# Kernel tuning notes

Measured on AMD Instinct MI355X. Metric: run time of the kernel, lower is better.

The kernel has to match this reference:

```python
import jax, jax.numpy as jnp
import numpy as np


def _lstm_cell(x, h, c, W_ih, W_hh, b_ih, b_hh):
    # torch gate order: input, forget, cell(g), output
    g = x @ W_ih.T + h @ W_hh.T + b_ih + b_hh
    i, f, gg, o = jnp.split(g, 4, axis=-1)
    c_new = jax.nn.sigmoid(f) * c + jax.nn.sigmoid(i) * jnp.tanh(gg)
    h_new = jax.nn.sigmoid(o) * jnp.tanh(c_new)
    return h_new, c_new


def setup_inputs() -> dict:
    key = jax.random.key(0)
    ks = jax.random.split(key, 11)
    T, B, D, E, H, V = 64, 4096, 32, 32, 5, 10
    IN = D + 3 * E  # 128 = input_size
    s = 0.1
    return {
        "horizon": T,
        "hidden": jax.random.normal(ks[0], (2, B, H), jnp.float32),
        "cell": jax.random.normal(ks[1], (2, B, H), jnp.float32),
        "dec_x": jax.random.normal(ks[2], (T, B, D), jnp.float32),
        "mote_id_cat": jax.random.randint(ks[3], (T, B), 0, V),
        "fault_type_cat": jax.random.randint(ks[4], (T, B), 0, V),
        "mote_fault_cat": jax.random.randint(ks[5], (T, B), 0, V),
        "mote_embed": jax.random.normal(ks[6], (V, E), jnp.float32),
        "W_ih0": jax.random.normal(ks[7], (4 * H, IN), jnp.float32) * s,
        "W_hh0": jax.random.normal(ks[8], (4 * H, H), jnp.float32) * s,
        "b_ih0": jnp.zeros((4 * H,), jnp.float32),
        "b_hh0": jnp.zeros((4 * H,), jnp.float32),
        "W_ih1": jax.random.normal(ks[9], (4 * H, H), jnp.float32) * s,
        "W_hh1": jax.random.normal(ks[10], (4 * H, H), jnp.float32) * s,
        "b_ih1": jnp.zeros((4 * H,), jnp.float32),
        "b_hh1": jnp.zeros((4 * H,), jnp.float32),
    }


def reference(horizon, hidden, cell, dec_x, mote_id_cat, fault_type_cat,
              mote_fault_cat, mote_embed, W_ih0, W_hh0, b_ih0, b_hh0,
              W_ih1, W_hh1, b_ih1, b_hh1):
    # Faithful to source: ALL three categorical features use mote_embed.
    e1 = mote_embed[mote_id_cat]      # [T,B,E]
    e2 = mote_embed[fault_type_cat]   # [T,B,E]
    e3 = mote_embed[mote_fault_cat]   # [T,B,E]
    x = jnp.concatenate([dec_x, e1, e2, e3], axis=-1)[:horizon]  # [T,B,IN]

    # Source re-feeds the SAME initial (hidden, cell) at every horizon step,
    # so steps are independent -> vmap over time (no carried recurrence).
    def step(xt):  # xt: [B, IN]
        h1, _ = _lstm_cell(xt, hidden[0], cell[0], W_ih0, W_hh0, b_ih0, b_hh0)
        h2, _ = _lstm_cell(h1, hidden[1], cell[1], W_ih1, W_hh1, b_ih1, b_hh1)
        return h2  # top-layer output, [B, H]

    return jax.vmap(step)(x)  # [T, B, H]
```

## Files before the change

### kernel.cpp

```cpp
#include <hip/hip_runtime.h>
#include <math.h>

#define HDIM 5
#define GATES 20
#define DDIM 32
#define EDIM 32
#define INDIM 128
#define VOC 10
#define SPN (3 * VOC * GATES)
#define HH_OFF 1024

__device__ __forceinline__ float sigmoidf_(float x) {
    return __builtin_amdgcn_rcpf(1.0f + __expf(-x));
}
__device__ __forceinline__ float tanhf_(float x) {
    float e = __expf(-2.0f * x);
    return fmaf(2.0f, __builtin_amdgcn_rcpf(1.0f + e), -1.0f);
}

__global__ __launch_bounds__(256) void precompute_kernel(
    const float* __restrict__ hidden,
    const float* __restrict__ emb,
    const float* __restrict__ W_ih0,
    const float* __restrict__ W_hh0, const float* __restrict__ b_ih0,
    const float* __restrict__ b_hh0,
    const float* __restrict__ W_hh1, const float* __restrict__ b_ih1,
    const float* __restrict__ b_hh1,
    float* __restrict__ ws, int B)
{
    int gid = blockIdx.x * 256 + threadIdx.x;
    if (gid < SPN) {
        int s = gid / (VOC * GATES);
        int rem = gid % (VOC * GATES);
        int v = rem / GATES, r = rem % GATES;
        const float4* ev = (const float4*)(emb + v * EDIM);
        const float4* wv = (const float4*)(W_ih0 + r * INDIM + DDIM + s * EDIM);
        float a = 0.0f;
        #pragma unroll
        for (int k = 0; k < EDIM / 4; ++k) {
            float4 e4 = ev[k], w4 = wv[k];
            a = fmaf(e4.x, w4.x, a); a = fmaf(e4.y, w4.y, a);
            a = fmaf(e4.z, w4.z, a); a = fmaf(e4.w, w4.w, a);
        }
        ws[gid] = a;
    }
    if (gid < B) {
        float h0[HDIM], h1v[HDIM];
        #pragma unroll
        for (int h = 0; h < HDIM; ++h) {
            h0[h]  = hidden[(size_t)gid * HDIM + h];
            h1v[h] = hidden[((size_t)B + gid) * HDIM + h];
        }
        #pragma unroll
        for (int r = 0; r < GATES; ++r) {
            float a0 = b_ih0[r] + b_hh0[r];
            float a1 = b_ih1[r] + b_hh1[r];
            #pragma unroll
            for (int h = 0; h < HDIM; ++h) {
                a0 = fmaf(h0[h],  W_hh0[r * HDIM + h], a0);
                a1 = fmaf(h1v[h], W_hh1[r * HDIM + h], a1);
            }
            ws[HH_OFF + (size_t)r * B + gid] = a0;
            ws[HH_OFF + (size_t)(GATES + r) * B + gid] = a1;
        }
    }
}

__global__ __launch_bounds__(256, 4) void decoder_kernel(
    const float* __restrict__ cell,
    const float* __restrict__ dec_x,
    const int*   __restrict__ midc,
    const int*   __restrict__ ftc,
    const int*   __restrict__ mfc,
    const float* __restrict__ W_ih0,
    const float* __restrict__ W_ih1,
    const float* __restrict__ ws,
    float* __restrict__ out,
    int B)
{
    const int b = blockIdx.x * 256 + threadIdx.x;
    if (b >= B) return;
    const int t = blockIdx.y;
    const size_t idx = (size_t)t * B + b;

    const float4* xp = (const float4*)(dec_x + idx * DDIM);
    float4 x[DDIM / 4];
    #pragma unroll
    for (int k = 0; k < DDIM / 4; ++k) x[k] = xp[k];

    const int vm = midc[idx], vf = ftc[idx], vmf = mfc[idx];

    float acc[GATES];
    const float* hh0 = ws + HH_OFF;
    #pragma unroll
    for (int r = 0; r < GATES; ++r) acc[r] = hh0[(size_t)r * B + b];

    const float4* P0 = (const float4*)(ws + vm * GATES);
    const float4* P1 = (const float4*)(ws + VOC * GATES + vf * GATES);
    const float4* P2 = (const float4*)(ws + 2 * VOC * GATES + vmf * GATES);
    #pragma unroll
    for (int k = 0; k < 5; ++k) {
        float4 p0 = P0[k], p1 = P1[k], p2 = P2[k];
        acc[4 * k + 0] += p0.x + p1.x + p2.x;
        acc[4 * k + 1] += p0.y + p1.y + p2.y;
        acc[4 * k + 2] += p0.z + p1.z + p2.z;
        acc[4 * k + 3] += p0.w + p1.w + p2.w;
    }

    #pragma unroll
    for (int r = 0; r < GATES; ++r) {
        const float* w = W_ih0 + r * INDIM;
        float a = acc[r];
        #pragma unroll
        for (int k = 0; k < DDIM / 4; ++k) {
            a = fmaf(x[k].x, w[4 * k + 0], a);
            a = fmaf(x[k].y, w[4 * k + 1], a);
            a = fmaf(x[k].z, w[4 * k + 2], a);
            a = fmaf(x[k].w, w[4 * k + 3], a);
        }
        acc[r] = a;
    }

    float h1[HDIM];
    #pragma unroll
    for (int r = 0; r < HDIM; ++r) {
        float c0 = cell[(size_t)b * HDIM + r];
        float ii = sigmoidf_(acc[r]);
        float ff = sigmoidf_(acc[HDIM + r]);
        float gg = tanhf_(acc[2 * HDIM + r]);
        float oo = sigmoidf_(acc[3 * HDIM + r]);
        float cn = fmaf(ff, c0, ii * gg);
        h1[r] = oo * tanhf_(cn);
    }

    float g1[GATES];
    const float* hh1 = ws + HH_OFF + (size_t)GATES * B;
    #pragma unroll
    for (int r = 0; r < GATES; ++r) {
        float a = hh1[(size_t)r * B + b];
        #pragma unroll
        for (int h = 0; h < HDIM; ++h)
            a = fmaf(h1[h], W_ih1[r * HDIM + h], a);
        g1[r] = a;
    }

    #pragma unroll
    for (int r = 0; r < HDIM; ++r) {
        float c1 = cell[((size_t)B + b) * HDIM + r];
        float ii = sigmoidf_(g1[r]);
        float ff = sigmoidf_(g1[HDIM + r]);
        float gg = tanhf_(g1[2 * HDIM + r]);
        float oo = sigmoidf_(g1[3 * HDIM + r]);
        float cn = fmaf(ff, c1, ii * gg);
        out[idx * HDIM + r] = oo * tanhf_(cn);
    }
}

extern "C" void kernel_launch(void* const* d_in, const int* in_sizes, int n_in,
                              void* d_out, int out_size, void* d_ws, size_t ws_size,
                              hipStream_t stream) {
    const float* hidden = (const float*)d_in[1];
    const float* cellp  = (const float*)d_in[2];
    const float* dec_x  = (const float*)d_in[3];
    const int*   midc   = (const int*)d_in[4];
    const int*   ftc    = (const int*)d_in[5];
    const int*   mfc    = (const int*)d_in[6];
    const float* emb    = (const float*)d_in[7];
    const float* W_ih0  = (const float*)d_in[8];
    const float* W_hh0  = (const float*)d_in[9];
    const float* b_ih0  = (const float*)d_in[10];
    const float* b_hh0  = (const float*)d_in[11];
    const float* W_ih1  = (const float*)d_in[12];
    const float* W_hh1  = (const float*)d_in[13];
    const float* b_ih1  = (const float*)d_in[14];
    const float* b_hh1  = (const float*)d_in[15];
    float* out = (float*)d_out;
    float* ws  = (float*)d_ws;

    int B = in_sizes[1] / (2 * HDIM);
    int horizon = out_size / (B * HDIM);

    int pre_n = (B > SPN ? B : SPN);
    int pre_grid = (pre_n + 255) / 256;
    precompute_kernel<<<pre_grid, 256, 0, stream>>>(
        hidden, emb, W_ih0, W_hh0, b_ih0, b_hh0, W_hh1, b_ih1, b_hh1, ws, B);

    dim3 grid((B + 255) / 256, horizon, 1);
    decoder_kernel<<<grid, 256, 0, stream>>>(
        cellp, dec_x, midc, ftc, mfc, W_ih0, W_ih1, ws, out, B);
}
```

Measured before the change: 121.3 us.

## Coalesce decoder loads and stores through LDS staging and transpose cell state

Stages each block's dec_x rows into padded shared memory with coalesced float4 loads, and stages outputs through shared memory so the global writes are contiguous. Copies the small embedding-projection table into LDS and moves the cell state into a gate-major workspace layout during precompute, so per-thread loads become coalesced. The aim is to fix strided per-thread global access in a memory-bound kernel. The cost is extra shared memory (about 37 KB per block), which may lower occupancy, plus two barriers.

```diff
diff --git a/kernel.cpp b/kernel.cpp
--- a/kernel.cpp
+++ b/kernel.cpp
@@ -9,6 +9,7 @@
 #define VOC 10
 #define SPN (3 * VOC * GATES)
 #define HH_OFF 1024
+#define ROWF4 9
 
 __device__ __forceinline__ float sigmoidf_(float x) {
     return __builtin_amdgcn_rcpf(1.0f + __expf(-x));
@@ -20,6 +21,7 @@
 
 __global__ __launch_bounds__(256) void precompute_kernel(
     const float* __restrict__ hidden,
+    const float* __restrict__ cell,
     const float* __restrict__ emb,
     const float* __restrict__ W_ih0,
     const float* __restrict__ W_hh0, const float* __restrict__ b_ih0,
@@ -63,11 +65,16 @@
             ws[HH_OFF + (size_t)r * B + gid] = a0;
             ws[HH_OFF + (size_t)(GATES + r) * B + gid] = a1;
         }
+        float* ct = ws + HH_OFF + (size_t)(2 * GATES) * B;
+        #pragma unroll
+        for (int r = 0; r < 2 * HDIM; ++r) {
+            int l = r / HDIM, rr = r % HDIM;
+            ct[(size_t)r * B + gid] = cell[((size_t)l * B + gid) * HDIM + rr];
+        }
     }
 }
 
 __global__ __launch_bounds__(256, 4) void decoder_kernel(
-    const float* __restrict__ cell,
     const float* __restrict__ dec_x,
     const int*   __restrict__ midc,
     const int*   __restrict__ ftc,
@@ -78,81 +85,116 @@
     float* __restrict__ out,
     int B)
 {
-    const int b = blockIdx.x * 256 + threadIdx.x;
-    if (b >= B) return;
-    const int t = blockIdx.y;
-    const size_t idx = (size_t)t * B + b;
-
-    const float4* xp = (const float4*)(dec_x + idx * DDIM);
+    __shared__ float4 sX[256 * ROWF4];
+    __shared__ float  sP[SPN];
+
+    const int tid = threadIdx.x;
+    const int b0  = blockIdx.x * 256;
+    const int b   = b0 + tid;
+    const int t   = blockIdx.y;
+    const bool valid = (b < B);
+    const int nb = (B - b0 < 256) ? (B - b0) : 256;
+
+    for (int j = tid; j < SPN; j += 256) sP[j] = ws[j];
+
+    const float4* gx = (const float4*)(dec_x + ((size_t)t * B + b0) * DDIM);
+    #pragma unroll
+    for (int j = 0; j < 8; ++j) {
+        int i = tid + 256 * j;
+        int row = i >> 3, col = i & 7;
+        if (row < nb) sX[row * ROWF4 + col] = gx[i];
+    }
+    __syncthreads();
+
     float4 x[DDIM / 4];
     #pragma unroll
-    for (int k = 0; k < DDIM / 4; ++k) x[k] = xp[k];
-
-    const int vm = midc[idx], vf = ftc[idx], vmf = mfc[idx];
-
-    float acc[GATES];
-    const float* hh0 = ws + HH_OFF;
+    for (int k = 0; k < DDIM / 4; ++k) x[k] = sX[tid * ROWF4 + k];
+
+    float h2[HDIM];
+    if (valid) {
+        const size_t idx = (size_t)t * B + b;
+        const int vm = midc[idx], vf = ftc[idx], vmf = mfc[idx];
+
+        float acc[GATES];
+        const float* hh0 = ws + HH_OFF;
+        #pragma unroll
+        for (int r = 0; r < GATES; ++r) acc[r] = hh0[(size_t)r * B + b];
+
+        const float4* P0 = (const float4*)(sP + vm * GATES);
+        const float4* P1 = (const float4*)(sP + VOC * GATES + vf * GATES);
+        const float4* P2 = (const float4*)(sP + 2 * VOC * GATES + vmf * GATES);
+        #pragma unroll
+        for (int k = 0; k < 5; ++k) {
+            float4 p0 = P0[k], p1 = P1[k], p2 = P2[k];
+            acc[4 * k + 0] += p0.x + p1.x + p2.x;
+            acc[4 * k + 1] += p0.y + p1.y + p2.y;
+            acc[4 * k + 2] += p0.z + p1.z + p2.z;
+            acc[4 * k + 3] += p0.w + p1.w + p2.w;
+        }
+
+        #pragma unroll
+        for (int r = 0; r < GATES; ++r) {
+            const float* w = W_ih0 + r * INDIM;
+            float a = acc[r];
+            #pragma unroll
+            for (int k = 0; k < DDIM / 4; ++k) {
+                a = fmaf(x[k].x, w[4 * k + 0], a);
+                a = fmaf(x[k].y, w[4 * k + 1], a);
+                a = fmaf(x[k].z, w[4 * k + 2], a);
+                a = fmaf(x[k].w, w[4 * k + 3], a);
+            }
+            acc[r] = a;
+        }
+
+        const float* ct = ws + HH_OFF + (size_t)(2 * GATES) * B;
+        float h1[HDIM];
+        #pragma unroll
+        for (int r = 0; r < HDIM; ++r) {
+            float c0 = ct[(size_t)r * B + b];
+            float ii = sigmoidf_(acc[r]);
+            float ff = sigmoidf_(acc[HDIM + r]);
+            float gg = tanhf_(acc[2 * HDIM + r]);
+            float oo = sigmoidf_(acc[3 * HDIM + r]);
+            float cn = fmaf(ff, c0, ii * gg);
+            h1[r] = oo * tanhf_(cn);
+        }
+
+        float g1[GATES];
+        const float* hh1 = ws + HH_OFF + (size_t)GATES * B;
+        #pragma unroll
+        for (int r = 0; r < GATES; ++r) {
+            float a = hh1[(size_t)r * B + b];
+            #pragma unroll
+            for (int h = 0; h < HDIM; ++h)
+                a = fmaf(h1[h], W_ih1[r * HDIM + h], a);
+            g1[r] = a;
+        }
+
+        #pragma unroll
+        for (int r = 0; r < HDIM; ++r) {
+            float c1 = ct[(size_t)(HDIM + r) * B + b];
+            float ii = sigmoidf_(g1[r]);
+            float ff = sigmoidf_(g1[HDIM + r]);
+            float gg = tanhf_(g1[2 * HDIM + r]);
+            float oo = sigmoidf_(g1[3 * HDIM + r]);
+            float cn = fmaf(ff, c1, ii * gg);
+            h2[r] = oo * tanhf_(cn);
+        }
+    }
+
+    __syncthreads();
+    float* sOut = (float*)sX;
+    if (valid) {
+        #pragma unroll
+        for (int r = 0; r < HDIM; ++r) sOut[tid * HDIM + r] = h2[r];
+    }
+    __syncthreads();
+    float* gout = out + ((size_t)t * B + b0) * HDIM;
+    const int cnt = nb * HDIM;
     #pragma unroll
-    for (int r = 0; r < GATES; ++r) acc[r] = hh0[(size_t)r * B + b];
-
-    const float4* P0 = (const float4*)(ws + vm * GATES);
-    const float4* P1 = (const float4*)(ws + VOC * GATES + vf * GATES);
-    const float4* P2 = (const float4*)(ws + 2 * VOC * GATES + vmf * GATES);
-    #pragma unroll
-    for (int k = 0; k < 5; ++k) {
-        float4 p0 = P0[k], p1 = P1[k], p2 = P2[k];
-        acc[4 * k + 0] += p0.x + p1.x + p2.x;
-        acc[4 * k + 1] += p0.y + p1.y + p2.y;
-        acc[4 * k + 2] += p0.z + p1.z + p2.z;
-        acc[4 * k + 3] += p0.w + p1.w + p2.w;
-    }
-
-    #pragma unroll
-    for (int r = 0; r < GATES; ++r) {
-        const float* w = W_ih0 + r * INDIM;
-        float a = acc[r];
-        #pragma unroll
-        for (int k = 0; k < DDIM / 4; ++k) {
-            a = fmaf(x[k].x, w[4 * k + 0], a);
-            a = fmaf(x[k].y, w[4 * k + 1], a);
-            a = fmaf(x[k].z, w[4 * k + 2], a);
-            a = fmaf(x[k].w, w[4 * k + 3], a);
-        }
-        acc[r] = a;
-    }
-
-    float h1[HDIM];
-    #pragma unroll
-    for (int r = 0; r < HDIM; ++r) {
-        float c0 = cell[(size_t)b * HDIM + r];
-        float ii = sigmoidf_(acc[r]);
-        float ff = sigmoidf_(acc[HDIM + r]);
-        float gg = tanhf_(acc[2 * HDIM + r]);
-        float oo = sigmoidf_(acc[3 * HDIM + r]);
-        float cn = fmaf(ff, c0, ii * gg);
-        h1[r] = oo * tanhf_(cn);
-    }
-
-    float g1[GATES];
-    const float* hh1 = ws + HH_OFF + (size_t)GATES * B;
-    #pragma unroll
-    for (int r = 0; r < GATES; ++r) {
-        float a = hh1[(size_t)r * B + b];
-        #pragma unroll
-        for (int h = 0; h < HDIM; ++h)
-            a = fmaf(h1[h], W_ih1[r * HDIM + h], a);
-        g1[r] = a;
-    }
-
-    #pragma unroll
-    for (int r = 0; r < HDIM; ++r) {
-        float c1 = cell[((size_t)B + b) * HDIM + r];
-        float ii = sigmoidf_(g1[r]);
-        float ff = sigmoidf_(g1[HDIM + r]);
-        float gg = tanhf_(g1[2 * HDIM + r]);
-        float oo = sigmoidf_(g1[3 * HDIM + r]);
-        float cn = fmaf(ff, c1, ii * gg);
-        out[idx * HDIM + r] = oo * tanhf_(cn);
+    for (int j = 0; j < HDIM; ++j) {
+        int i = j * 256 + tid;
+        if (i < cnt) gout[i] = sOut[i];
     }
 }
 
@@ -183,9 +225,10 @@
     int pre_n = (B > SPN ? B : SPN);
     int pre_grid = (pre_n + 255) / 256;
     precompute_kernel<<<pre_grid, 256, 0, stream>>>(
-        hidden, emb, W_ih0, W_hh0, b_ih0, b_hh0, W_hh1, b_ih1, b_hh1, ws, B);
+        hidden, cellp, emb, W_ih0, W_hh0, b_ih0, b_hh0, W_hh1, b_ih1, b_hh1,
+        ws, B);
 
     dim3 grid((B + 255) / 256, horizon, 1);
     decoder_kernel<<<grid, 256, 0, stream>>>(
-        cellp, dec_x, midc, ftc, mfc, W_ih0, W_ih1, ws, out, B);
-}
+        dec_x, midc, ftc, mfc, W_ih0, W_ih1, ws, out, B);
+}
```

New measurement: 121.1 us. Within noise of the previous version (-0.1%).
